# Kernel tuning notes

Hardware: AMD Instinct MI355X
Metric: run time of the kernel (lower is better)

The kernel has to match this reference:

```python
import jax, jax.numpy as jnp
import numpy as np

VEC_SIZE = 128
N_VECS = 8
N_ROWS = 256  # n_choices * redundancy
BATCH = 512
EPS = 1e-8


def _combos(n):
    # combos[i, j] = 0 if bit j of i is set else 1  -> shape [2^n, n]
    i = np.arange(2 ** n)[:, None]
    j = np.arange(n)[None, :]
    return jnp.asarray(((i >> j) & 1) == 0, dtype=jnp.float32)


def setup_inputs() -> dict:
    key = jax.random.key(0)
    kq, kw = jax.random.split(key)
    query = jax.random.normal(kq, (BATCH, N_VECS * VEC_SIZE), dtype=jnp.float32)
    weight = jax.random.normal(kw, (N_ROWS, N_VECS * VEC_SIZE), dtype=jnp.float32)
    # match torch init: weight rows normalized over full flattened dim
    weight = weight / jnp.clip(jnp.linalg.norm(weight, axis=1, keepdims=True), EPS)
    return {"query": query, "weight": weight}


def reference(query, weight):
    combos = _combos(N_VECS)                               # [C, n]  C = 2^n
    q = query.reshape(-1, N_VECS, VEC_SIZE)                # [b, n, v]
    w = weight.reshape(-1, N_VECS, VEC_SIZE)               # [r, n, v]
    # cosine similarity over vec_size, per (batch row, weight row, vec slot)
    dot = jnp.einsum('bnv,rnv->brn', q, w)                 # [b, r, n]
    qn = jnp.maximum(jnp.linalg.norm(q, axis=-1), EPS)     # [b, n]
    wn = jnp.maximum(jnp.linalg.norm(w, axis=-1), EPS)     # [r, n]
    cos_sim = dot / (qn[:, None, :] * wn[None, :, :])
    cos_sim = jax.nn.relu(cos_sim)                         # [b, r, n]
    # NAND combo interpolation then product over the n_vecs axis
    cs = cos_sim[:, :, None, :]                            # [b, r, 1, n]
    c = combos[None, None, :, :]                           # [1, 1, C, n]
    transformed = c * cs + (1.0 - c) * (1.0 - cs)          # [b, r, C, n]
    return jnp.prod(transformed, axis=-1)                  # [b, r, C]
```

## Files before the change

### kernel.cpp

```cpp
#include <hip/hip_runtime.h>
#include <math.h>

#define BATCH  512
#define NROWS  256
#define NVECS  8
#define VSIZE  128
#define DIM    1024
#define NCOMBO 256

typedef float vf4 __attribute__((ext_vector_type(4)));

__global__ __launch_bounds__(256) void fused_kernel(
    const float* __restrict__ q, const float* __restrict__ w,
    float* __restrict__ out) {
  __shared__ __align__(16) float Ws[8 * 1056];
  __shared__ __align__(16) float CS[64][8];
  const int t  = threadIdx.x;
  const int wv = t >> 6, lane = t & 63;
  const int bs = blockIdx.x * 8, rs = blockIdx.y * 8;

  #pragma unroll
  for (int i = 0; i < 8; ++i) {
    int f = i * 256 + t;
    int g = f << 2;
    int row = g >> 10, e = g & 1023;
    float4 v = *(const float4*)(w + (size_t)(rs + row) * DIM + e);
    *(float4*)(Ws + row * 1056 + (e >> 7) * 132 + (e & 127)) = v;
  }

  const int n = lane >> 3, c = lane & 7;
  const int koff = n * VSIZE + c * 16;

  float4 qa[4], qb[4];
  float qs0 = 0.f, qs1 = 0.f;
  {
    const float* Q0 = q + (size_t)(bs + 2 * wv) * DIM + koff;
    #pragma unroll
    for (int j = 0; j < 4; ++j) {
      qa[j] = *(const float4*)(Q0 + 4 * j);
      qb[j] = *(const float4*)(Q0 + DIM + 4 * j);
      qs0 = fmaf(qa[j].x, qa[j].x, qs0); qs0 = fmaf(qa[j].y, qa[j].y, qs0);
      qs0 = fmaf(qa[j].z, qa[j].z, qs0); qs0 = fmaf(qa[j].w, qa[j].w, qs0);
      qs1 = fmaf(qb[j].x, qb[j].x, qs1); qs1 = fmaf(qb[j].y, qb[j].y, qs1);
      qs1 = fmaf(qb[j].z, qb[j].z, qs1); qs1 = fmaf(qb[j].w, qb[j].w, qs1);
    }
  }
  #pragma unroll
  for (int m = 1; m <= 4; m <<= 1) {
    qs0 += __shfl_xor(qs0, m, 64);
    qs1 += __shfl_xor(qs1, m, 64);
  }
  const float iq0 = 1.0f / fmaxf(sqrtf(qs0), 1e-8f);
  const float iq1 = 1.0f / fmaxf(sqrtf(qs1), 1e-8f);
  __syncthreads();

  const float* Wb = Ws + n * 132 + c * 16;
  #pragma unroll
  for (int r = 0; r < 8; ++r) {
    const float* Wr = Wb + r * 1056;
    float s0 = 0.f, s1 = 0.f, wss = 0.f;
    #pragma unroll
    for (int j = 0; j < 4; ++j) {
      float4 w4 = *(const float4*)(Wr + 4 * j);
      s0 = fmaf(qa[j].x, w4.x, s0); s0 = fmaf(qa[j].y, w4.y, s0);
      s0 = fmaf(qa[j].z, w4.z, s0); s0 = fmaf(qa[j].w, w4.w, s0);
      s1 = fmaf(qb[j].x, w4.x, s1); s1 = fmaf(qb[j].y, w4.y, s1);
      s1 = fmaf(qb[j].z, w4.z, s1); s1 = fmaf(qb[j].w, w4.w, s1);
      wss = fmaf(w4.x, w4.x, wss); wss = fmaf(w4.y, w4.y, wss);
      wss = fmaf(w4.z, w4.z, wss); wss = fmaf(w4.w, w4.w, wss);
    }
    #pragma unroll
    for (int m = 1; m <= 4; m <<= 1) {
      s0  += __shfl_xor(s0, m, 64);
      s1  += __shfl_xor(s1, m, 64);
      wss += __shfl_xor(wss, m, 64);
    }
    const float iw = 1.0f / fmaxf(sqrtf(wss), 1e-8f);
    if (c < 2) {
      float v = (c == 0) ? s0 * iq0 * iw : s1 * iq1 * iw;
      CS[(2 * wv + c) * 8 + r][n] = fmaxf(v, 0.f);
    }
  }
  __syncthreads();

  #pragma unroll 4
  for (int i = 0; i < 16; ++i) {
    int p = wv * 16 + i;
    int bl = p >> 3, r = p & 7;
    float4 cA = *(const float4*)(&CS[p][0]);
    float4 cB = *(const float4*)(&CS[p][4]);
    float t2 = (lane & 1)  ? 1.f - cA.z : cA.z;
    float t3 = (lane & 2)  ? 1.f - cA.w : cA.w;
    float t4 = (lane & 4)  ? 1.f - cB.x : cB.x;
    float t5 = (lane & 8)  ? 1.f - cB.y : cB.y;
    float t6 = (lane & 16) ? 1.f - cB.z : cB.z;
    float t7 = (lane & 32) ? 1.f - cB.w : cB.w;
    float base = ((t2 * t3) * (t4 * t5)) * (t6 * t7);
    float c0 = cA.x, c1 = cA.y;
    float4 o;
    o.x = base * (c0 * c1);
    o.y = base * ((1.f - c0) * c1);
    o.z = base * (c0 * (1.f - c1));
    o.w = base * ((1.f - c0) * (1.f - c1));
    size_t off = ((size_t)(bs + bl) * NROWS + (rs + r)) * NCOMBO + lane * 4;
    *(float4*)(out + off) = o;
  }
}

extern "C" void kernel_launch(void* const* d_in, const int* in_sizes, int n_in,
                              void* d_out, int out_size, void* d_ws, size_t ws_size,
                              hipStream_t stream) {
  const float* query  = (const float*)d_in[0];
  const float* weight = (const float*)d_in[1];
  float* out = (float*)d_out;
  (void)d_ws; (void)ws_size;

  hipLaunchKernelGGL(fused_kernel, dim3(64, 32), dim3(256), 0, stream,
                     query, weight, out);
}
```

Measured before the change: 145.5 us.

## Drop LDS staging and barriers; read weights from global, broadcast cosines via shuffles

Removes the shared-memory staging of the weight tile and both __syncthreads barriers. Each wave now reads its weight rows straight from global memory (L2-cached across blocks) and passes the per-slot cosine values to all lanes with wavefront shuffles instead of an LDS scratch buffer. Output is written per row inside the r loop. This trades LDS use and sync latency for redundant global/L2 reads of weights across the four waves, plus extra shuffle instructions.

```diff
diff --git a/kernel.cpp b/kernel.cpp
--- a/kernel.cpp
+++ b/kernel.cpp
@@ -8,33 +8,20 @@
 #define DIM    1024
 #define NCOMBO 256
 
-typedef float vf4 __attribute__((ext_vector_type(4)));
-
 __global__ __launch_bounds__(256) void fused_kernel(
     const float* __restrict__ q, const float* __restrict__ w,
     float* __restrict__ out) {
-  __shared__ __align__(16) float Ws[8 * 1056];
-  __shared__ __align__(16) float CS[64][8];
-  const int t  = threadIdx.x;
-  const int wv = t >> 6, lane = t & 63;
-  const int bs = blockIdx.x * 8, rs = blockIdx.y * 8;
-
-  #pragma unroll
-  for (int i = 0; i < 8; ++i) {
-    int f = i * 256 + t;
-    int g = f << 2;
-    int row = g >> 10, e = g & 1023;
-    float4 v = *(const float4*)(w + (size_t)(rs + row) * DIM + e);
-    *(float4*)(Ws + row * 1056 + (e >> 7) * 132 + (e & 127)) = v;
-  }
-
-  const int n = lane >> 3, c = lane & 7;
+  const int t    = threadIdx.x;
+  const int wv   = t >> 6, lane = t & 63;
+  const int bs   = blockIdx.x * 8, rs = blockIdx.y * 8;
+  const int n    = lane >> 3, c = lane & 7;
   const int koff = n * VSIZE + c * 16;
+  const int b0   = bs + 2 * wv;
 
   float4 qa[4], qb[4];
   float qs0 = 0.f, qs1 = 0.f;
   {
-    const float* Q0 = q + (size_t)(bs + 2 * wv) * DIM + koff;
+    const float* Q0 = q + (size_t)b0 * DIM + koff;
     #pragma unroll
     for (int j = 0; j < 4; ++j) {
       qa[j] = *(const float4*)(Q0 + 4 * j);
@@ -52,12 +39,13 @@
   }
   const float iq0 = 1.0f / fmaxf(sqrtf(qs0), 1e-8f);
   const float iq1 = 1.0f / fmaxf(sqrtf(qs1), 1e-8f);
-  __syncthreads();
 
-  const float* Wb = Ws + n * 132 + c * 16;
-  #pragma unroll
+  const float* Wbase = w + (size_t)rs * DIM + koff;
+  float* out0 = out + ((size_t)b0 * NROWS + rs) * NCOMBO + lane * 4;
+
+  #pragma unroll 2
   for (int r = 0; r < 8; ++r) {
-    const float* Wr = Wb + r * 1056;
+    const float* Wr = Wbase + r * DIM;
     float s0 = 0.f, s1 = 0.f, wss = 0.f;
     #pragma unroll
     for (int j = 0; j < 4; ++j) {
@@ -75,35 +63,35 @@
       s1  += __shfl_xor(s1, m, 64);
       wss += __shfl_xor(wss, m, 64);
     }
-    const float iw = 1.0f / fmaxf(sqrtf(wss), 1e-8f);
-    if (c < 2) {
-      float v = (c == 0) ? s0 * iq0 * iw : s1 * iq1 * iw;
-      CS[(2 * wv + c) * 8 + r][n] = fmaxf(v, 0.f);
+    const float iw  = 1.0f / fmaxf(sqrtf(wss), 1e-8f);
+    const float cs0 = fmaxf(s0 * iq0 * iw, 0.f);
+    const float cs1 = fmaxf(s1 * iq1 * iw, 0.f);
+
+    float v0[8], v1[8];
+    #pragma unroll
+    for (int j = 0; j < 8; ++j) {
+      v0[j] = __shfl(cs0, j * 8, 64);
+      v1[j] = __shfl(cs1, j * 8, 64);
     }
-  }
-  __syncthreads();
 
-  #pragma unroll 4
-  for (int i = 0; i < 16; ++i) {
-    int p = wv * 16 + i;
-    int bl = p >> 3, r = p & 7;
-    float4 cA = *(const float4*)(&CS[p][0]);
-    float4 cB = *(const float4*)(&CS[p][4]);
-    float t2 = (lane & 1)  ? 1.f - cA.z : cA.z;
-    float t3 = (lane & 2)  ? 1.f - cA.w : cA.w;
-    float t4 = (lane & 4)  ? 1.f - cB.x : cB.x;
-    float t5 = (lane & 8)  ? 1.f - cB.y : cB.y;
-    float t6 = (lane & 16) ? 1.f - cB.z : cB.z;
-    float t7 = (lane & 32) ? 1.f - cB.w : cB.w;
-    float base = ((t2 * t3) * (t4 * t5)) * (t6 * t7);
-    float c0 = cA.x, c1 = cA.y;
-    float4 o;
-    o.x = base * (c0 * c1);
-    o.y = base * ((1.f - c0) * c1);
-    o.z = base * (c0 * (1.f - c1));
-    o.w = base * ((1.f - c0) * (1.f - c1));
-    size_t off = ((size_t)(bs + bl) * NROWS + (rs + r)) * NCOMBO + lane * 4;
-    *(float4*)(out + off) = o;
+    #pragma unroll
+    for (int pp = 0; pp < 2; ++pp) {
+      const float* v = pp ? v1 : v0;
+      float t2 = (lane & 1)  ? 1.f - v[2] : v[2];
+      float t3 = (lane & 2)  ? 1.f - v[3] : v[3];
+      float t4 = (lane & 4)  ? 1.f - v[4] : v[4];
+      float t5 = (lane & 8)  ? 1.f - v[5] : v[5];
+      float t6 = (lane & 16) ? 1.f - v[6] : v[6];
+      float t7 = (lane & 32) ? 1.f - v[7] : v[7];
+      float base = ((t2 * t3) * (t4 * t5)) * (t6 * t7);
+      float c0 = v[0], c1 = v[1];
+      float4 o;
+      o.x = base * (c0 * c1);
+      o.y = base * ((1.f - c0) * c1);
+      o.z = base * (c0 * (1.f - c1));
+      o.w = base * ((1.f - c0) * (1.f - c1));
+      *(float4*)(out0 + ((size_t)pp * NROWS + r) * NCOMBO) = o;
+    }
   }
 }
 
```

Result: slower. 152.3 us (+4.7%).
